# Optimization experiments

Hardware: AMD Instinct MI355X
Metric: run time of the kernel (lower is better)

Reference implementation:

```python
import jax, jax.numpy as jnp
import numpy as np


def setup_inputs() -> dict:
    key = jax.random.key(0)
    k_x, k1, k2, k3 = jax.random.split(key, 4)
    dim, hidden, out_dim = 4096, 8192, 4096
    x = jax.random.normal(k_x, (4, 2048, dim), dtype=jnp.float32)
    # VNNILinear initializes weight = randn(out, in) * 0.02
    w1 = jax.random.normal(k1, (hidden, dim), dtype=jnp.float32) * 0.02
    w2 = jax.random.normal(k2, (out_dim, hidden), dtype=jnp.float32) * 0.02
    w3 = jax.random.normal(k3, (hidden, dim), dtype=jnp.float32) * 0.02
    return {"x": x, "w1": w1, "w2": w2, "w3": w3}


def _quant_linear(x, w):
    """Emulate VNNILinear int8 weight-quantized matmul (inference path).

    Per-output-channel symmetric quant: scale = max|w_row| / 127,
    w_q = round(w / scale) in int8, y = x @ (w_q * scale).T.
    """
    w_max = jnp.clip(jnp.max(jnp.abs(w), axis=1, keepdims=True), 1e-6)  # [out,1]
    scale_w = w_max / 127.0
    w_q = jnp.round(w / scale_w).astype(jnp.int8)
    w_dq = w_q.astype(jnp.float32) * scale_w  # dequantized weight
    return jnp.einsum('bsd,hd->bsh', x, w_dq)


def reference(x, w1, w2, w3):
    # SwiGLU: w2( silu(w1(x)) * w3(x) ), all bias-free, int8 VNNI weight quant
    h = jax.nn.silu(_quant_linear(x, w1)) * _quant_linear(x, w3)  # [B,S,hidden]
    return _quant_linear(h, w2)  # [B,S,out_dim]
```

## Files before the change

### kernel.cpp

```cpp
#include <hip/hip_runtime.h>
#include <hip/hip_bf16.h>
#include <stdint.h>


typedef short bf16x8 __attribute__((ext_vector_type(8)));
typedef float f32x4  __attribute__((ext_vector_type(4)));
typedef float f32x16 __attribute__((ext_vector_type(16)));
typedef int   i32x4  __attribute__((ext_vector_type(4)));
typedef int   i32x16 __attribute__((ext_vector_type(16)));

__device__ __forceinline__ unsigned short f2bf(float f) {
  unsigned u = __builtin_bit_cast(unsigned, f);
  u += 0x7FFFu + ((u >> 16) & 1u);
  return (unsigned short)(u >> 16);
}

#define GLOAD_LDS16(gaddr, laddr)                                             \
  __builtin_amdgcn_global_load_lds(                                           \
      (const __attribute__((address_space(1))) void*)(gaddr),                 \
      (__attribute__((address_space(3))) void*)(laddr), 16, 0, 0)

#define FENCE()      asm volatile("" ::: "memory")
#define BAR()        __builtin_amdgcn_s_barrier()
#define WAIT_LGKM(n) asm volatile("s_waitcnt lgkmcnt(" #n ")" ::: "memory")
#define WAIT_VM8()   asm volatile("s_waitcnt vmcnt(8)" ::: "memory")
#define WAIT_VM4()   asm volatile("s_waitcnt vmcnt(4)" ::: "memory")
#define WAIT_VM0()   asm volatile("s_waitcnt vmcnt(0)" ::: "memory")
#define SFENCE()     __builtin_amdgcn_sched_barrier(0)
#define PRIO1()      __builtin_amdgcn_s_setprio(1)
#define PRIO0()      __builtin_amdgcn_s_setprio(0)


__global__ void quant_rows_i8_kernel(const float* __restrict__ w,
                                     char* __restrict__ q,
                                     float* __restrict__ scale, int cols,
                                     float clip) {
  const int row = blockIdx.x;
  const float* wr = w + (size_t)row * cols;
  char* qr = q + (size_t)row * cols;

  float m = 0.f;
  for (int c = threadIdx.x * 4; c < cols; c += blockDim.x * 4) {
    float4 v = *reinterpret_cast<const float4*>(wr + c);
    m = fmaxf(m, fmaxf(fmaxf(fabsf(v.x), fabsf(v.y)),
                       fmaxf(fabsf(v.z), fabsf(v.w))));
  }
#pragma unroll
  for (int off = 32; off; off >>= 1) m = fmaxf(m, __shfl_xor(m, off));
  __shared__ float smax[4];
  if ((threadIdx.x & 63) == 0) smax[threadIdx.x >> 6] = m;
  __syncthreads();
  m = fmaxf(fmaxf(smax[0], smax[1]), fmaxf(smax[2], smax[3]));

  const float s = fmaxf(m, clip) / 127.0f;
  if (threadIdx.x == 0) scale[row] = s;
  for (int c = threadIdx.x * 4; c < cols; c += blockDim.x * 4) {
    float4 v = *reinterpret_cast<const float4*>(wr + c);
    int b0 = (int)rintf(v.x / s), b1 = (int)rintf(v.y / s);
    int b2 = (int)rintf(v.z / s), b3 = (int)rintf(v.w / s);
    unsigned pk = (b0 & 0xff) | ((b1 & 0xff) << 8) | ((b2 & 0xff) << 16)
                  | ((b3 & 0xff) << 24);
    *reinterpret_cast<unsigned*>(qr + c) = pk;
  }
}

__global__ void quant_rows_bf16_kernel(const float* __restrict__ w,
                                       unsigned short* __restrict__ wq,
                                       int cols) {
  const int row = blockIdx.x;
  const float* wr = w + (size_t)row * cols;
  unsigned short* wqr = wq + (size_t)row * cols;

  float m = 0.f;
  for (int c = threadIdx.x * 4; c < cols; c += blockDim.x * 4) {
    float4 v = *reinterpret_cast<const float4*>(wr + c);
    m = fmaxf(m, fmaxf(fmaxf(fabsf(v.x), fabsf(v.y)),
                       fmaxf(fabsf(v.z), fabsf(v.w))));
  }
#pragma unroll
  for (int off = 32; off; off >>= 1) m = fmaxf(m, __shfl_xor(m, off));
  __shared__ float smax[4];
  if ((threadIdx.x & 63) == 0) smax[threadIdx.x >> 6] = m;
  __syncthreads();
  m = fmaxf(fmaxf(smax[0], smax[1]), fmaxf(smax[2], smax[3]));

  const float s = fmaxf(m, 1e-6f) / 127.0f;
  for (int c = threadIdx.x * 4; c < cols; c += blockDim.x * 4) {
    float4 v = *reinterpret_cast<const float4*>(wr + c);
    ushort4 o;
    o.x = f2bf(rintf(v.x / s) * s);
    o.y = f2bf(rintf(v.y / s) * s);
    o.z = f2bf(rintf(v.z / s) * s);
    o.w = f2bf(rintf(v.w / s) * s);
    *reinterpret_cast<ushort4*>(wqr + c) = o;
  }
}


__device__ __forceinline__ void xcd_swizzle(int& bx, int& by, int gx, int gy) {
  int nwg = gx * gy;
  int bid = by * gx + bx;
  int cpx = nwg >> 3;
  int s = (bid & 7) * cpx + (bid >> 3);
  by = s / gx;
  bx = s % gx;
}

__global__ __launch_bounds__(512, 2)
void gemm_i8_swiglu_kernel(const char* __restrict__ Aq,
                           const char* __restrict__ B1q,
                           const char* __restrict__ B3q,
                           const float* __restrict__ sx,
                           const float* __restrict__ sw1,
                           const float* __restrict__ sw3,
                           unsigned short* __restrict__ H,
                           int M, int N, int K) {
  __shared__ alignas(1024) char lds[131072];

  int bx = blockIdx.x, by = blockIdx.y;
  xcd_swizzle(bx, by, gridDim.x, gridDim.y);
  const int brow = by * 256, bcol = bx * 128;

  const int t = threadIdx.x, lane = t & 63, w = t >> 6;
  const int wr = w >> 2, wc = w & 3;
  const int l31 = lane & 31, hi = lane >> 5;
  const int NT = K >> 6;

  const int rS = t >> 2;
  const int gcS = ((t & 3) ^ ((t >> 3) & 3)) * 16;
  const char* srcA  = Aq  + (size_t)(brow + rS) * K + gcS;
  const char* srcB1 = B1q + (size_t)(bcol + rS) * K + gcS;
  const char* srcB3 = B3q + (size_t)(bcol + rS) * K + gcS;

#define STAGE_A(kt)                                                           \
  {                                                                           \
    const int s2 = ((kt) & 3) * 32768;                                        \
    const size_t ko = (size_t)(kt) * 64;                                      \
    GLOAD_LDS16(srcA + ko, lds + s2 + t * 16);                                \
    GLOAD_LDS16(srcA + (size_t)128 * K + ko, lds + s2 + 8192 + t * 16);       \
  }
#define STAGE_B(kt)                                                           \
  {                                                                           \
    const int s2 = ((kt) & 3) * 32768;                                        \
    const size_t ko = (size_t)(kt) * 64;                                      \
    GLOAD_LDS16(srcB1 + ko, lds + s2 + 16384 + t * 16);                       \
    GLOAD_LDS16(srcB3 + ko, lds + s2 + 24576 + t * 16);                       \
  }

  STAGE_A(0); STAGE_B(0);
  STAGE_A(1); STAGE_B(1);
  STAGE_A(2); STAGE_B(2);
  WAIT_VM8();
  FENCE(); BAR();

  const int sx2 = (l31 >> 1) & 3;
  const int aoff  = (wr * 128 + l31) * 64 + ((hi ^ sx2) * 16);
  const int boff1 = 16384 + (wc * 32 + l31) * 64 + ((hi ^ sx2) * 16);
  const int boff3 = boff1 + 8192;

  i32x16 acc[4][2] = {};
  i32x4 a0[4], b10, b30;
  i32x4 a1[4], b11, b31;

#pragma unroll
  for (int m = 0; m < 4; ++m)
    a0[m] = *reinterpret_cast<const i32x4*>(lds + aoff + m * 2048);
  b10 = *reinterpret_cast<const i32x4*>(lds + boff1);
  b30 = *reinterpret_cast<const i32x4*>(lds + boff3);

#define MFMA8(ar, b1r, b3r)                                                   \
  acc[0][0] = __builtin_amdgcn_mfma_i32_32x32x32_i8(ar[0], b1r, acc[0][0], 0, 0, 0); \
  acc[0][1] = __builtin_amdgcn_mfma_i32_32x32x32_i8(ar[0], b3r, acc[0][1], 0, 0, 0); \
  acc[1][0] = __builtin_amdgcn_mfma_i32_32x32x32_i8(ar[1], b1r, acc[1][0], 0, 0, 0); \
  acc[1][1] = __builtin_amdgcn_mfma_i32_32x32x32_i8(ar[1], b3r, acc[1][1], 0, 0, 0); \
  acc[2][0] = __builtin_amdgcn_mfma_i32_32x32x32_i8(ar[2], b1r, acc[2][0], 0, 0, 0); \
  acc[2][1] = __builtin_amdgcn_mfma_i32_32x32x32_i8(ar[2], b3r, acc[2][1], 0, 0, 0); \
  acc[3][0] = __builtin_amdgcn_mfma_i32_32x32x32_i8(ar[3], b1r, acc[3][0], 0, 0, 0); \
  acc[3][1] = __builtin_amdgcn_mfma_i32_32x32x32_i8(ar[3], b3r, acc[3][1], 0, 0, 0)

  int kb = 0;
  for (; kb < NT - 4; kb += 4) {
    const char* pA  = srcA  + (size_t)kb * 64;
    const char* pB1 = srcB1 + (size_t)kb * 64;
    const char* pB3 = srcB3 + (size_t)kb * 64;
#pragma unroll
    for (int s = 0; s < 4; ++s) {
      const char* sl = lds + s * 32768;
      const char* sn = lds + (((s + 1) & 3) * 32768);
      char* sp = lds + (((s + 3) & 3) * 32768);
      const int ko = (s + 3) * 64;

      a1[0] = *reinterpret_cast<const i32x4*>(sl + (aoff ^ 32));
      a1[1] = *reinterpret_cast<const i32x4*>(sl + (aoff ^ 32) + 2048);
      a1[2] = *reinterpret_cast<const i32x4*>(sl + (aoff ^ 32) + 4096);
      a1[3] = *reinterpret_cast<const i32x4*>(sl + (aoff ^ 32) + 6144);
      b11 = *reinterpret_cast<const i32x4*>(sl + (boff1 ^ 32));
      b31 = *reinterpret_cast<const i32x4*>(sl + (boff3 ^ 32));
      GLOAD_LDS16(pA + ko, sp + t * 16);
      GLOAD_LDS16(pA + (size_t)128 * K + ko, sp + 8192 + t * 16);
      WAIT_LGKM(6); SFENCE();
      PRIO1(); MFMA8(a0, b10, b30); PRIO0();

      GLOAD_LDS16(pB1 + ko, sp + 16384 + t * 16);
      GLOAD_LDS16(pB3 + ko, sp + 24576 + t * 16);
      WAIT_VM8();
      WAIT_LGKM(0);
      FENCE(); BAR();
      a0[0] = *reinterpret_cast<const i32x4*>(sn + aoff);
      a0[1] = *reinterpret_cast<const i32x4*>(sn + aoff + 2048);
      a0[2] = *reinterpret_cast<const i32x4*>(sn + aoff + 4096);
      a0[3] = *reinterpret_cast<const i32x4*>(sn + aoff + 6144);
      b10 = *reinterpret_cast<const i32x4*>(sn + boff1);
      b30 = *reinterpret_cast<const i32x4*>(sn + boff3);
      SFENCE();
      PRIO1(); MFMA8(a1, b11, b31); PRIO0();
    }
  }

  for (int k = kb; k < NT; ++k) {
    const char* sl = lds + (k & 3) * 32768;
    const bool pf = (k + 3 < NT);

    a1[0] = *reinterpret_cast<const i32x4*>(sl + (aoff ^ 32));
    a1[1] = *reinterpret_cast<const i32x4*>(sl + (aoff ^ 32) + 2048);
    a1[2] = *reinterpret_cast<const i32x4*>(sl + (aoff ^ 32) + 4096);
    a1[3] = *reinterpret_cast<const i32x4*>(sl + (aoff ^ 32) + 6144);
    b11 = *reinterpret_cast<const i32x4*>(sl + (boff1 ^ 32));
    b31 = *reinterpret_cast<const i32x4*>(sl + (boff3 ^ 32));
    if (pf) STAGE_A(k + 3);
    WAIT_LGKM(6); SFENCE();
    PRIO1(); MFMA8(a0, b10, b30); PRIO0();

    if (pf) {
      STAGE_B(k + 3);
      WAIT_VM8();
    } else if (k == NT - 3) {
      WAIT_VM4();
    } else if (k == NT - 2) {
      WAIT_VM0();
    }
    WAIT_LGKM(0);
    FENCE(); BAR();
    if (k + 1 < NT) {
      const char* sn = lds + ((k + 1) & 3) * 32768;
      a0[0] = *reinterpret_cast<const i32x4*>(sn + aoff);
      a0[1] = *reinterpret_cast<const i32x4*>(sn + aoff + 2048);
      a0[2] = *reinterpret_cast<const i32x4*>(sn + aoff + 4096);
      a0[3] = *reinterpret_cast<const i32x4*>(sn + aoff + 6144);
      b10 = *reinterpret_cast<const i32x4*>(sn + boff1);
      b30 = *reinterpret_cast<const i32x4*>(sn + boff3);
    }
    SFENCE();
    PRIO1(); MFMA8(a1, b11, b31); PRIO0();
  }
#undef MFMA8
#undef STAGE_A
#undef STAGE_B

  const int ocol = bcol + wc * 32 + l31;
  const int rowb = brow + wr * 128 + 4 * hi;
  const float sw1c = sw1[ocol], sw3c = sw3[ocol];
#pragma unroll
  for (int m = 0; m < 4; ++m) {
#pragma unroll
    for (int rq = 0; rq < 4; ++rq) {
      const int r0 = rowb + m * 32 + 8 * rq;
      const f32x4 sx4 = *reinterpret_cast<const f32x4*>(sx + r0);
#pragma unroll
      for (int j = 0; j < 4; ++j) {
        float y1 = (float)acc[m][0][rq * 4 + j] * (sx4[j] * sw1c);
        float y3 = (float)acc[m][1][rq * 4 + j] * (sx4[j] * sw3c);
        float hv = (y1 / (1.f + __expf(-y1))) * y3;
        H[(size_t)(r0 + j) * N + ocol] = f2bf(hv);
      }
    }
  }
}

__global__ __launch_bounds__(512, 2)
void gemm_bf16_kernel(const unsigned short* __restrict__ A,
                      const unsigned short* __restrict__ B,
                      float* __restrict__ C, int M, int N, int K) {
  __shared__ alignas(1024) unsigned short lds[65536];

  int bx = blockIdx.x, by = blockIdx.y;
  xcd_swizzle(bx, by, gridDim.x, gridDim.y);
  const int brow = by * 256, bcol = bx * 256;

  const int t = threadIdx.x, lane = t & 63, w = t >> 6;
  const int wr = w >> 2, wc = w & 3;
  const int l31 = lane & 31, hi = lane >> 5;
  const int NT = K >> 5;

  const int rS = t >> 2;
  const int cS = ((t & 3) ^ ((t >> 3) & 3)) * 8;
  const unsigned short* srcA = A + (size_t)(brow + rS) * K + cS;
  const unsigned short* srcB = B + (size_t)(bcol + rS) * K + cS;

#define STAGE_A(kt)                                                           \
  {                                                                           \
    const int s2 = ((kt) & 3) * 16384;                                        \
    const size_t ko = (size_t)(kt) * 32;                                      \
    GLOAD_LDS16(srcA + ko, &lds[s2 + t * 8]);                                 \
    GLOAD_LDS16(srcA + (size_t)128 * K + ko, &lds[s2 + 4096 + t * 8]);        \
  }
#define STAGE_B(kt)                                                           \
  {                                                                           \
    const int s2 = ((kt) & 3) * 16384;                                        \
    const size_t ko = (size_t)(kt) * 32;                                      \
    GLOAD_LDS16(srcB + ko, &lds[s2 + 8192 + t * 8]);                          \
    GLOAD_LDS16(srcB + (size_t)128 * K + ko, &lds[s2 + 12288 + t * 8]);       \
  }

  STAGE_A(0); STAGE_B(0);
  STAGE_A(1); STAGE_B(1);
  STAGE_A(2); STAGE_B(2);
  WAIT_VM8();
  FENCE(); BAR();

  const int sx2 = (l31 >> 1) & 3;
  const int aoff  = (wr * 128 + l31) * 32 + ((hi ^ sx2) * 8);
  const int boff0 = 8192 + (wc * 64 + l31) * 32 + ((hi ^ sx2) * 8);

  f32x16 acc[4][2] = {};
  bf16x8 a0[4], b00, b01;
  bf16x8 a1[4], b10, b11;

#pragma unroll
  for (int m = 0; m < 4; ++m)
    a0[m] = *reinterpret_cast<const bf16x8*>(&lds[aoff + m * 1024]);
  b00 = *reinterpret_cast<const bf16x8*>(&lds[boff0]);
  b01 = *reinterpret_cast<const bf16x8*>(&lds[boff0 + 1024]);

#define MFMA8(ar, bx0, bx1)                                                   \
  acc[0][0] = __builtin_amdgcn_mfma_f32_32x32x16_bf16(ar[0], bx0, acc[0][0], 0, 0, 0); \
  acc[0][1] = __builtin_amdgcn_mfma_f32_32x32x16_bf16(ar[0], bx1, acc[0][1], 0, 0, 0); \
  acc[1][0] = __builtin_amdgcn_mfma_f32_32x32x16_bf16(ar[1], bx0, acc[1][0], 0, 0, 0); \
  acc[1][1] = __builtin_amdgcn_mfma_f32_32x32x16_bf16(ar[1], bx1, acc[1][1], 0, 0, 0); \
  acc[2][0] = __builtin_amdgcn_mfma_f32_32x32x16_bf16(ar[2], bx0, acc[2][0], 0, 0, 0); \
  acc[2][1] = __builtin_amdgcn_mfma_f32_32x32x16_bf16(ar[2], bx1, acc[2][1], 0, 0, 0); \
  acc[3][0] = __builtin_amdgcn_mfma_f32_32x32x16_bf16(ar[3], bx0, acc[3][0], 0, 0, 0); \
  acc[3][1] = __builtin_amdgcn_mfma_f32_32x32x16_bf16(ar[3], bx1, acc[3][1], 0, 0, 0)

  int kb = 0;
  for (; kb < NT - 4; kb += 4) {
    const unsigned short* pA = srcA + (size_t)kb * 32;
    const unsigned short* pB = srcB + (size_t)kb * 32;
#pragma unroll
    for (int s = 0; s < 4; ++s) {
      const unsigned short* sl = lds + s * 16384;
      const unsigned short* sn = lds + (((s + 1) & 3) * 16384);
      unsigned short* sp = lds + (((s + 3) & 3) * 16384);
      const int ko = (s + 3) * 32;

      a1[0] = *reinterpret_cast<const bf16x8*>(sl + (aoff ^ 16));
      a1[1] = *reinterpret_cast<const bf16x8*>(sl + (aoff ^ 16) + 1024);
      a1[2] = *reinterpret_cast<const bf16x8*>(sl + (aoff ^ 16) + 2048);
      a1[3] = *reinterpret_cast<const bf16x8*>(sl + (aoff ^ 16) + 3072);
      b10 = *reinterpret_cast<const bf16x8*>(sl + (boff0 ^ 16));
      b11 = *reinterpret_cast<const bf16x8*>(sl + ((boff0 + 1024) ^ 16));
      GLOAD_LDS16(pA + ko, sp + t * 8);
      GLOAD_LDS16(pA + (size_t)128 * K + ko, sp + 4096 + t * 8);
      WAIT_LGKM(6); SFENCE();
      PRIO1(); MFMA8(a0, b00, b01); PRIO0();

      GLOAD_LDS16(pB + ko, sp + 8192 + t * 8);
      GLOAD_LDS16(pB + (size_t)128 * K + ko, sp + 12288 + t * 8);
      WAIT_VM8();
      WAIT_LGKM(0);
      FENCE(); BAR();
      a0[0] = *reinterpret_cast<const bf16x8*>(sn + aoff);
      a0[1] = *reinterpret_cast<const bf16x8*>(sn + aoff + 1024);
      a0[2] = *reinterpret_cast<const bf16x8*>(sn + aoff + 2048);
      a0[3] = *reinterpret_cast<const bf16x8*>(sn + aoff + 3072);
      b00 = *reinterpret_cast<const bf16x8*>(sn + boff0);
      b01 = *reinterpret_cast<const bf16x8*>(sn + boff0 + 1024);
      SFENCE();
      PRIO1(); MFMA8(a1, b10, b11); PRIO0();
    }
  }

  for (int k = kb; k < NT; ++k) {
    const unsigned short* sl = &lds[(k & 3) * 16384];
    const bool pf = (k + 3 < NT);

    a1[0] = *reinterpret_cast<const bf16x8*>(sl + (aoff ^ 16));
    a1[1] = *reinterpret_cast<const bf16x8*>(sl + (aoff ^ 16) + 1024);
    a1[2] = *reinterpret_cast<const bf16x8*>(sl + (aoff ^ 16) + 2048);
    a1[3] = *reinterpret_cast<const bf16x8*>(sl + (aoff ^ 16) + 3072);
    b10 = *reinterpret_cast<const bf16x8*>(sl + (boff0 ^ 16));
    b11 = *reinterpret_cast<const bf16x8*>(sl + ((boff0 + 1024) ^ 16));
    if (pf) STAGE_A(k + 3);
    WAIT_LGKM(6); SFENCE();
    PRIO1(); MFMA8(a0, b00, b01); PRIO0();

    if (pf) {
      STAGE_B(k + 3);
      WAIT_VM8();
    } else if (k == NT - 3) {
      WAIT_VM4();
    } else if (k == NT - 2) {
      WAIT_VM0();
    }
    WAIT_LGKM(0);
    FENCE(); BAR();
    if (k + 1 < NT) {
      const unsigned short* sn = &lds[((k + 1) & 3) * 16384];
      a0[0] = *reinterpret_cast<const bf16x8*>(sn + aoff);
      a0[1] = *reinterpret_cast<const bf16x8*>(sn + aoff + 1024);
      a0[2] = *reinterpret_cast<const bf16x8*>(sn + aoff + 2048);
      a0[3] = *reinterpret_cast<const bf16x8*>(sn + aoff + 3072);
      b00 = *reinterpret_cast<const bf16x8*>(sn + boff0);
      b01 = *reinterpret_cast<const bf16x8*>(sn + boff0 + 1024);
    }
    SFENCE();
    PRIO1(); MFMA8(a1, b10, b11); PRIO0();
  }
#undef MFMA8
#undef STAGE_A
#undef STAGE_B

  const int ocol = bcol + wc * 64 + l31;
  const int rowb = brow + wr * 128 + 4 * hi;
#pragma unroll
  for (int m = 0; m < 4; ++m)
#pragma unroll
    for (int n = 0; n < 2; ++n)
#pragma unroll
      for (int rq = 0; rq < 4; ++rq)
#pragma unroll
        for (int j = 0; j < 4; ++j)
          C[(size_t)(rowb + m * 32 + 8 * rq + j) * N + (ocol + n * 32)] =
              acc[m][n][rq * 4 + j];
}


extern "C" void kernel_launch(void* const* d_in, const int* in_sizes, int n_in,
                              void* d_out, int out_size, void* d_ws,
                              size_t ws_size, hipStream_t stream) {
  const float* x  = (const float*)d_in[0];
  const float* w1 = (const float*)d_in[1];
  const float* w2 = (const float*)d_in[2];
  const float* w3 = (const float*)d_in[3];
  float* out = (float*)d_out;

  const int DIM = 4096, HID = 8192;
  const int M = in_sizes[0] / DIM;

  char* xq  = (char*)d_ws;
  char* w1q = xq + (size_t)M * DIM;
  char* w3q = w1q + (size_t)HID * DIM;
  unsigned short* w2b = (unsigned short*)(w3q + (size_t)HID * DIM);
  unsigned short* h = w2b + (size_t)DIM * HID;
  float* sx  = (float*)(h + (size_t)M * HID);
  float* sw1 = sx + M;
  float* sw3 = sw1 + HID;

  quant_rows_i8_kernel<<<HID, 256, 0, stream>>>(w1, w1q, sw1, DIM, 1e-6f);
  quant_rows_i8_kernel<<<HID, 256, 0, stream>>>(w3, w3q, sw3, DIM, 1e-6f);
  quant_rows_i8_kernel<<<M, 256, 0, stream>>>(x, xq, sx, DIM, 1e-30f);
  quant_rows_bf16_kernel<<<DIM, 256, 0, stream>>>(w2, w2b, HID);

  gemm_i8_swiglu_kernel<<<dim3(HID / 128, M / 256), 512, 0, stream>>>(
      xq, w1q, w3q, sx, sw1, sw3, h, M, HID, DIM);
  gemm_bf16_kernel<<<dim3(DIM / 256, M / 256), 512, 0, stream>>>(
      h, w2b, out, M, DIM, HID);
}
```

Before: 1.235 ms.

## Hold quant rows in registers; balance GEMM staging loads across waves; stagger k-halves

The quantization kernels now load each row once into registers and reuse it for both the max pass and the quantize pass, removing the second global read of the fp32 weights and activations. In both GEMM kernels, odd and even waves swap which operand (A or B) they stage in the first and second prefetch slots, which evens out global-load issue between the two halves of each iteration. Odd waves also read the two k-halves of each LDS stage in the opposite order, likely to spread LDS bank traffic. The changes add template specialisation on fixed column counts and a per-wave branch in the staging code.

```diff
diff --git a/kernel.cpp b/kernel.cpp
--- a/kernel.cpp
+++ b/kernel.cpp
@@ -31,19 +31,21 @@
 #define PRIO0()      __builtin_amdgcn_s_setprio(0)
 
 
-__global__ void quant_rows_i8_kernel(const float* __restrict__ w,
-                                     char* __restrict__ q,
-                                     float* __restrict__ scale, int cols,
-                                     float clip) {
-  const int row = blockIdx.x;
-  const float* wr = w + (size_t)row * cols;
-  char* qr = q + (size_t)row * cols;
-
+template <int NCH>
+__global__ void quant_rows_i8_sp(const float* __restrict__ w,
+                                 char* __restrict__ q,
+                                 float* __restrict__ scale, float clip) {
+  const int cols = NCH * 1024;
+  const float* wr = w + (size_t)blockIdx.x * cols;
+  char* qr = q + (size_t)blockIdx.x * cols;
+
+  float4 v[NCH];
   float m = 0.f;
-  for (int c = threadIdx.x * 4; c < cols; c += blockDim.x * 4) {
-    float4 v = *reinterpret_cast<const float4*>(wr + c);
-    m = fmaxf(m, fmaxf(fmaxf(fabsf(v.x), fabsf(v.y)),
-                       fmaxf(fabsf(v.z), fabsf(v.w))));
+#pragma unroll
+  for (int j = 0; j < NCH; ++j) {
+    v[j] = *reinterpret_cast<const float4*>(wr + threadIdx.x * 4 + j * 1024);
+    m = fmaxf(m, fmaxf(fmaxf(fabsf(v[j].x), fabsf(v[j].y)),
+                       fmaxf(fabsf(v[j].z), fabsf(v[j].w))));
   }
 #pragma unroll
   for (int off = 32; off; off >>= 1) m = fmaxf(m, __shfl_xor(m, off));
@@ -53,29 +55,31 @@
   m = fmaxf(fmaxf(smax[0], smax[1]), fmaxf(smax[2], smax[3]));
 
   const float s = fmaxf(m, clip) / 127.0f;
-  if (threadIdx.x == 0) scale[row] = s;
-  for (int c = threadIdx.x * 4; c < cols; c += blockDim.x * 4) {
-    float4 v = *reinterpret_cast<const float4*>(wr + c);
-    int b0 = (int)rintf(v.x / s), b1 = (int)rintf(v.y / s);
-    int b2 = (int)rintf(v.z / s), b3 = (int)rintf(v.w / s);
+  if (threadIdx.x == 0) scale[blockIdx.x] = s;
+#pragma unroll
+  for (int j = 0; j < NCH; ++j) {
+    int b0 = (int)rintf(v[j].x / s), b1 = (int)rintf(v[j].y / s);
+    int b2 = (int)rintf(v[j].z / s), b3 = (int)rintf(v[j].w / s);
     unsigned pk = (b0 & 0xff) | ((b1 & 0xff) << 8) | ((b2 & 0xff) << 16)
                   | ((b3 & 0xff) << 24);
-    *reinterpret_cast<unsigned*>(qr + c) = pk;
-  }
-}
-
-__global__ void quant_rows_bf16_kernel(const float* __restrict__ w,
-                                       unsigned short* __restrict__ wq,
-                                       int cols) {
-  const int row = blockIdx.x;
-  const float* wr = w + (size_t)row * cols;
-  unsigned short* wqr = wq + (size_t)row * cols;
-
+    *reinterpret_cast<unsigned*>(qr + threadIdx.x * 4 + j * 1024) = pk;
+  }
+}
+
+template <int NCH>
+__global__ void quant_rows_bf16_sp(const float* __restrict__ w,
+                                   unsigned short* __restrict__ wq) {
+  const int cols = NCH * 1024;
+  const float* wr = w + (size_t)blockIdx.x * cols;
+  unsigned short* wqr = wq + (size_t)blockIdx.x * cols;
+
+  float4 v[NCH];
   float m = 0.f;
-  for (int c = threadIdx.x * 4; c < cols; c += blockDim.x * 4) {
-    float4 v = *reinterpret_cast<const float4*>(wr + c);
-    m = fmaxf(m, fmaxf(fmaxf(fabsf(v.x), fabsf(v.y)),
-                       fmaxf(fabsf(v.z), fabsf(v.w))));
+#pragma unroll
+  for (int j = 0; j < NCH; ++j) {
+    v[j] = *reinterpret_cast<const float4*>(wr + threadIdx.x * 4 + j * 1024);
+    m = fmaxf(m, fmaxf(fmaxf(fabsf(v[j].x), fabsf(v[j].y)),
+                       fmaxf(fabsf(v[j].z), fabsf(v[j].w))));
   }
 #pragma unroll
   for (int off = 32; off; off >>= 1) m = fmaxf(m, __shfl_xor(m, off));
@@ -85,14 +89,14 @@
   m = fmaxf(fmaxf(smax[0], smax[1]), fmaxf(smax[2], smax[3]));
 
   const float s = fmaxf(m, 1e-6f) / 127.0f;
-  for (int c = threadIdx.x * 4; c < cols; c += blockDim.x * 4) {
-    float4 v = *reinterpret_cast<const float4*>(wr + c);
+#pragma unroll
+  for (int j = 0; j < NCH; ++j) {
     ushort4 o;
-    o.x = f2bf(rintf(v.x / s) * s);
-    o.y = f2bf(rintf(v.y / s) * s);
-    o.z = f2bf(rintf(v.z / s) * s);
-    o.w = f2bf(rintf(v.w / s) * s);
-    *reinterpret_cast<ushort4*>(wqr + c) = o;
+    o.x = f2bf(rintf(v[j].x / s) * s);
+    o.y = f2bf(rintf(v[j].y / s) * s);
+    o.z = f2bf(rintf(v[j].z / s) * s);
+    o.w = f2bf(rintf(v[j].w / s) * s);
+    *reinterpret_cast<ushort4*>(wqr + threadIdx.x * 4 + j * 1024) = o;
   }
 }
 
@@ -124,6 +128,7 @@
   const int t = threadIdx.x, lane = t & 63, w = t >> 6;
   const int wr = w >> 2, wc = w & 3;
   const int l31 = lane & 31, hi = lane >> 5;
+  const bool wodd = (w & 1);
   const int NT = K >> 6;
 
   const int rS = t >> 2;
@@ -132,24 +137,29 @@
   const char* srcB1 = B1q + (size_t)(bcol + rS) * K + gcS;
   const char* srcB3 = B3q + (size_t)(bcol + rS) * K + gcS;
 
-#define STAGE_A(kt)                                                           \
-  {                                                                           \
-    const int s2 = ((kt) & 3) * 32768;                                        \
-    const size_t ko = (size_t)(kt) * 64;                                      \
-    GLOAD_LDS16(srcA + ko, lds + s2 + t * 16);                                \
-    GLOAD_LDS16(srcA + (size_t)128 * K + ko, lds + s2 + 8192 + t * 16);       \
-  }
-#define STAGE_B(kt)                                                           \
-  {                                                                           \
-    const int s2 = ((kt) & 3) * 32768;                                        \
-    const size_t ko = (size_t)(kt) * 64;                                      \
-    GLOAD_LDS16(srcB1 + ko, lds + s2 + 16384 + t * 16);                       \
-    GLOAD_LDS16(srcB3 + ko, lds + s2 + 24576 + t * 16);                       \
-  }
-
-  STAGE_A(0); STAGE_B(0);
-  STAGE_A(1); STAGE_B(1);
-  STAGE_A(2); STAGE_B(2);
+#define STAGE_P1(pA_, pB1_, pB3_, sp, ko)                                     \
+  if (!wodd) {                                                                \
+    GLOAD_LDS16((pA_) + (ko), (sp) + t * 16);                                 \
+    GLOAD_LDS16((pA_) + (size_t)128 * K + (ko), (sp) + 8192 + t * 16);        \
+  } else {                                                                    \
+    GLOAD_LDS16((pB1_) + (ko), (sp) + 16384 + t * 16);                        \
+    GLOAD_LDS16((pB3_) + (ko), (sp) + 24576 + t * 16);                        \
+  }
+#define STAGE_P2(pA_, pB1_, pB3_, sp, ko)                                     \
+  if (wodd) {                                                                 \
+    GLOAD_LDS16((pA_) + (ko), (sp) + t * 16);                                 \
+    GLOAD_LDS16((pA_) + (size_t)128 * K + (ko), (sp) + 8192 + t * 16);        \
+  } else {                                                                    \
+    GLOAD_LDS16((pB1_) + (ko), (sp) + 16384 + t * 16);                        \
+    GLOAD_LDS16((pB3_) + (ko), (sp) + 24576 + t * 16);                        \
+  }
+
+  STAGE_P1(srcA, srcB1, srcB3, lds, 0);
+  STAGE_P2(srcA, srcB1, srcB3, lds, 0);
+  STAGE_P1(srcA, srcB1, srcB3, lds + 32768, (size_t)64);
+  STAGE_P2(srcA, srcB1, srcB3, lds + 32768, (size_t)64);
+  STAGE_P1(srcA, srcB1, srcB3, lds + 65536, (size_t)128);
+  STAGE_P2(srcA, srcB1, srcB3, lds + 65536, (size_t)128);
   WAIT_VM8();
   FENCE(); BAR();
 
@@ -157,6 +167,8 @@
   const int aoff  = (wr * 128 + l31) * 64 + ((hi ^ sx2) * 16);
   const int boff1 = 16384 + (wc * 32 + l31) * 64 + ((hi ^ sx2) * 16);
   const int boff3 = boff1 + 8192;
+  const int kx0 = wodd ? 32 : 0;
+  const int kx1 = kx0 ^ 32;
 
   i32x16 acc[4][2] = {};
   i32x4 a0[4], b10, b30;
@@ -164,9 +176,9 @@
 
 #pragma unroll
   for (int m = 0; m < 4; ++m)
-    a0[m] = *reinterpret_cast<const i32x4*>(lds + aoff + m * 2048);
-  b10 = *reinterpret_cast<const i32x4*>(lds + boff1);
-  b30 = *reinterpret_cast<const i32x4*>(lds + boff3);
+    a0[m] = *reinterpret_cast<const i32x4*>(lds + (aoff ^ kx0) + m * 2048);
+  b10 = *reinterpret_cast<const i32x4*>(lds + (boff1 ^ kx0));
+  b30 = *reinterpret_cast<const i32x4*>(lds + (boff3 ^ kx0));
 
 #define MFMA8(ar, b1r, b3r)                                                   \
   acc[0][0] = __builtin_amdgcn_mfma_i32_32x32x32_i8(ar[0], b1r, acc[0][0], 0, 0, 0); \
@@ -190,28 +202,26 @@
       char* sp = lds + (((s + 3) & 3) * 32768);
       const int ko = (s + 3) * 64;
 
-      a1[0] = *reinterpret_cast<const i32x4*>(sl + (aoff ^ 32));
-      a1[1] = *reinterpret_cast<const i32x4*>(sl + (aoff ^ 32) + 2048);
-      a1[2] = *reinterpret_cast<const i32x4*>(sl + (aoff ^ 32) + 4096);
-      a1[3] = *reinterpret_cast<const i32x4*>(sl + (aoff ^ 32) + 6144);
-      b11 = *reinterpret_cast<const i32x4*>(sl + (boff1 ^ 32));
-      b31 = *reinterpret_cast<const i32x4*>(sl + (boff3 ^ 32));
-      GLOAD_LDS16(pA + ko, sp + t * 16);
-      GLOAD_LDS16(pA + (size_t)128 * K + ko, sp + 8192 + t * 16);
+      a1[0] = *reinterpret_cast<const i32x4*>(sl + (aoff ^ kx1));
+      a1[1] = *reinterpret_cast<const i32x4*>(sl + (aoff ^ kx1) + 2048);
+      a1[2] = *reinterpret_cast<const i32x4*>(sl + (aoff ^ kx1) + 4096);
+      a1[3] = *reinterpret_cast<const i32x4*>(sl + (aoff ^ kx1) + 6144);
+      b11 = *reinterpret_cast<const i32x4*>(sl + (boff1 ^ kx1));
+      b31 = *reinterpret_cast<const i32x4*>(sl + (boff3 ^ kx1));
+      STAGE_P1(pA, pB1, pB3, sp, ko);
       WAIT_LGKM(6); SFENCE();
       PRIO1(); MFMA8(a0, b10, b30); PRIO0();
 
-      GLOAD_LDS16(pB1 + ko, sp + 16384 + t * 16);
-      GLOAD_LDS16(pB3 + ko, sp + 24576 + t * 16);
+      STAGE_P2(pA, pB1, pB3, sp, ko);
       WAIT_VM8();
       WAIT_LGKM(0);
       FENCE(); BAR();
-      a0[0] = *reinterpret_cast<const i32x4*>(sn + aoff);
-      a0[1] = *reinterpret_cast<const i32x4*>(sn + aoff + 2048);
-      a0[2] = *reinterpret_cast<const i32x4*>(sn + aoff + 4096);
-      a0[3] = *reinterpret_cast<const i32x4*>(sn + aoff + 6144);
-      b10 = *reinterpret_cast<const i32x4*>(sn + boff1);
-      b30 = *reinterpret_cast<const i32x4*>(sn + boff3);
+      a0[0] = *reinterpret_cast<const i32x4*>(sn + (aoff ^ kx0));
+      a0[1] = *reinterpret_cast<const i32x4*>(sn + (aoff ^ kx0) + 2048);
+      a0[2] = *reinterpret_cast<const i32x4*>(sn + (aoff ^ kx0) + 4096);
+      a0[3] = *reinterpret_cast<const i32x4*>(sn + (aoff ^ kx0) + 6144);
+      b10 = *reinterpret_cast<const i32x4*>(sn + (boff1 ^ kx0));
+      b30 = *reinterpret_cast<const i32x4*>(sn + (boff3 ^ kx0));
       SFENCE();
       PRIO1(); MFMA8(a1, b11, b31); PRIO0();
     }
@@ -221,18 +231,22 @@
     const char* sl = lds + (k & 3) * 32768;
     const bool pf = (k + 3 < NT);
 
-    a1[0] = *reinterpret_cast<const i32x4*>(sl + (aoff ^ 32));
-    a1[1] = *reinterpret_cast<const i32x4*>(sl + (aoff ^ 32) + 2048);
-    a1[2] = *reinterpret_cast<const i32x4*>(sl + (aoff ^ 32) + 4096);
-    a1[3] = *reinterpret_cast<const i32x4*>(sl + (aoff ^ 32) + 6144);
-    b11 = *reinterpret_cast<const i32x4*>(sl + (boff1 ^ 32));
-    b31 = *reinterpret_cast<const i32x4*>(sl + (boff3 ^ 32));
-    if (pf) STAGE_A(k + 3);
+    a1[0] = *reinterpret_cast<const i32x4*>(sl + (aoff ^ kx1));
+    a1[1] = *reinterpret_cast<const i32x4*>(sl + (aoff ^ kx1) + 2048);
+    a1[2] = *reinterpret_cast<const i32x4*>(sl + (aoff ^ kx1) + 4096);
+    a1[3] = *reinterpret_cast<const i32x4*>(sl + (aoff ^ kx1) + 6144);
+    b11 = *reinterpret_cast<const i32x4*>(sl + (boff1 ^ kx1));
+    b31 = *reinterpret_cast<const i32x4*>(sl + (boff3 ^ kx1));
+    if (pf) {
+      char* sp = lds + (((k + 3) & 3) * 32768);
+      STAGE_P1(srcA, srcB1, srcB3, sp, (size_t)(k + 3) * 64);
+    }
     WAIT_LGKM(6); SFENCE();
     PRIO1(); MFMA8(a0, b10, b30); PRIO0();
 
     if (pf) {
-      STAGE_B(k + 3);
+      char* sp = lds + (((k + 3) & 3) * 32768);
+      STAGE_P2(srcA, srcB1, srcB3, sp, (size_t)(k + 3) * 64);
       WAIT_VM8();
     } else if (k == NT - 3) {
       WAIT_VM4();
@@ -243,19 +257,19 @@
     FENCE(); BAR();
     if (k + 1 < NT) {
       const char* sn = lds + ((k + 1) & 3) * 32768;
-      a0[0] = *reinterpret_cast<const i32x4*>(sn + aoff);
-      a0[1] = *reinterpret_cast<const i32x4*>(sn + aoff + 2048);
-      a0[2] = *reinterpret_cast<const i32x4*>(sn + aoff + 4096);
-      a0[3] = *reinterpret_cast<const i32x4*>(sn + aoff + 6144);
-      b10 = *reinterpret_cast<const i32x4*>(sn + boff1);
-      b30 = *reinterpret_cast<const i32x4*>(sn + boff3);
+      a0[0] = *reinterpret_cast<const i32x4*>(sn + (aoff ^ kx0));
+      a0[1] = *reinterpret_cast<const i32x4*>(sn + (aoff ^ kx0) + 2048);
+      a0[2] = *reinterpret_cast<const i32x4*>(sn + (aoff ^ kx0) + 4096);
+      a0[3] = *reinterpret_cast<const i32x4*>(sn + (aoff ^ kx0) + 6144);
+      b10 = *reinterpret_cast<const i32x4*>(sn + (boff1 ^ kx0));
+      b30 = *reinterpret_cast<const i32x4*>(sn + (boff3 ^ kx0));
     }
     SFENCE();
     PRIO1(); MFMA8(a1, b11, b31); PRIO0();
   }
 #undef MFMA8
-#undef STAGE_A
-#undef STAGE_B
+#undef STAGE_P1
+#undef STAGE_P2
 
   const int ocol = bcol + wc * 32 + l31;
   const int rowb = brow + wr * 128 + 4 * hi;
@@ -290,6 +304,7 @@
   const int t = threadIdx.x, lane = t & 63, w = t >> 6;
   const int wr = w >> 2, wc = w & 3;
   const int l31 = lane & 31, hi = lane >> 5;
+  const bool wodd = (w & 1);
   const int NT = K >> 5;
 
   const int rS = t >> 2;
@@ -297,30 +312,38 @@
   const unsigned short* srcA = A + (size_t)(brow + rS) * K + cS;
   const unsigned short* srcB = B + (size_t)(bcol + rS) * K + cS;
 
-#define STAGE_A(kt)                                                           \
-  {                                                                           \
-    const int s2 = ((kt) & 3) * 16384;                                        \
-    const size_t ko = (size_t)(kt) * 32;                                      \
-    GLOAD_LDS16(srcA + ko, &lds[s2 + t * 8]);                                 \
-    GLOAD_LDS16(srcA + (size_t)128 * K + ko, &lds[s2 + 4096 + t * 8]);        \
-  }
-#define STAGE_B(kt)                                                           \
-  {                                                                           \
-    const int s2 = ((kt) & 3) * 16384;                                        \
-    const size_t ko = (size_t)(kt) * 32;                                      \
-    GLOAD_LDS16(srcB + ko, &lds[s2 + 8192 + t * 8]);                          \
-    GLOAD_LDS16(srcB + (size_t)128 * K + ko, &lds[s2 + 12288 + t * 8]);       \
-  }
-
-  STAGE_A(0); STAGE_B(0);
-  STAGE_A(1); STAGE_B(1);
-  STAGE_A(2); STAGE_B(2);
+#define STAGE_P1(pA_, pB_, sp, ko)                                            \
+  if (!wodd) {                                                                \
+    GLOAD_LDS16((pA_) + (ko), (sp) + t * 8);                                  \
+    GLOAD_LDS16((pA_) + (size_t)128 * K + (ko), (sp) + 4096 + t * 8);         \
+  } else {                                                                    \
+    GLOAD_LDS16((pB_) + (ko), (sp) + 8192 + t * 8);                           \
+    GLOAD_LDS16((pB_) + (size_t)128 * K + (ko), (sp) + 12288 + t * 8);        \
+  }
+#define STAGE_P2(pA_, pB_, sp, ko)                                            \
+  if (wodd) {                                                                 \
+    GLOAD_LDS16((pA_) + (ko), (sp) + t * 8);                                  \
+    GLOAD_LDS16((pA_) + (size_t)128 * K + (ko), (sp) + 4096 + t * 8);         \
+  } else {                                                                    \
+    GLOAD_LDS16((pB_) + (ko), (sp) + 8192 + t * 8);                           \
+    GLOAD_LDS16((pB_) + (size_t)128 * K + (ko), (sp) + 12288 + t * 8);        \
+  }
+
+  STAGE_P1(srcA, srcB, lds, 0);
+  STAGE_P2(srcA, srcB, lds, 0);
+  STAGE_P1(srcA, srcB, lds + 16384, (size_t)32);
+  STAGE_P2(srcA, srcB, lds + 16384, (size_t)32);
+  STAGE_P1(srcA, srcB, lds + 32768, (size_t)64);
+  STAGE_P2(srcA, srcB, lds + 32768, (size_t)64);
   WAIT_VM8();
   FENCE(); BAR();
 
   const int sx2 = (l31 >> 1) & 3;
   const int aoff  = (wr * 128 + l31) * 32 + ((hi ^ sx2) * 8);
   const int boff0 = 8192 + (wc * 64 + l31) * 32 + ((hi ^ sx2) * 8);
+  const int boff1b = boff0 + 1024;
+  const int kx0 = wodd ? 16 : 0;
+  const int kx1 = kx0 ^ 16;
 
   f32x16 acc[4][2] = {};
   bf16x8 a0[4], b00, b01;
@@ -328,9 +351,9 @@
 
 #pragma unroll
   for (int m = 0; m < 4; ++m)
-    a0[m] = *reinterpret_cast<const bf16x8*>(&lds[aoff + m * 1024]);
-  b00 = *reinterpret_cast<const bf16x8*>(&lds[boff0]);
-  b01 = *reinterpret_cast<const bf16x8*>(&lds[boff0 + 1024]);
+    a0[m] = *reinterpret_cast<const bf16x8*>(&lds[(aoff ^ kx0) + m * 1024]);
+  b00 = *reinterpret_cast<const bf16x8*>(&lds[boff0 ^ kx0]);
+  b01 = *reinterpret_cast<const bf16x8*>(&lds[boff1b ^ kx0]);
 
 #define MFMA8(ar, bx0, bx1)                                                   \
   acc[0][0] = __builtin_amdgcn_mfma_f32_32x32x16_bf16(ar[0], bx0, acc[0][0], 0, 0, 0); \
@@ -353,28 +376,26 @@
       unsigned short* sp = lds + (((s + 3) & 3) * 16384);
       const int ko = (s + 3) * 32;
 
-      a1[0] = *reinterpret_cast<const bf16x8*>(sl + (aoff ^ 16));
-      a1[1] = *reinterpret_cast<const bf16x8*>(sl + (aoff ^ 16) + 1024);
-      a1[2] = *reinterpret_cast<const bf16x8*>(sl + (aoff ^ 16) + 2048);
-      a1[3] = *reinterpret_cast<const bf16x8*>(sl + (aoff ^ 16) + 3072);
-      b10 = *reinterpret_cast<const bf16x8*>(sl + (boff0 ^ 16));
-      b11 = *reinterpret_cast<const bf16x8*>(sl + ((boff0 + 1024) ^ 16));
-      GLOAD_LDS16(pA + ko, sp + t * 8);
-      GLOAD_LDS16(pA + (size_t)128 * K + ko, sp + 4096 + t * 8);
+      a1[0] = *reinterpret_cast<const bf16x8*>(sl + (aoff ^ kx1));
+      a1[1] = *reinterpret_cast<const bf16x8*>(sl + (aoff ^ kx1) + 1024);
+      a1[2] = *reinterpret_cast<const bf16x8*>(sl + (aoff ^ kx1) + 2048);
+      a1[3] = *reinterpret_cast<const bf16x8*>(sl + (aoff ^ kx1) + 3072);
+      b10 = *reinterpret_cast<const bf16x8*>(sl + (boff0 ^ kx1));
+      b11 = *reinterpret_cast<const bf16x8*>(sl + (boff1b ^ kx1));
+      STAGE_P1(pA, pB, sp, ko);
       WAIT_LGKM(6); SFENCE();
       PRIO1(); MFMA8(a0, b00, b01); PRIO0();
 
-      GLOAD_LDS16(pB + ko, sp + 8192 + t * 8);
-      GLOAD_LDS16(pB + (size_t)128 * K + ko, sp + 12288 + t * 8);
+      STAGE_P2(pA, pB, sp, ko);
       WAIT_VM8();
       WAIT_LGKM(0);
       FENCE(); BAR();
-      a0[0] = *reinterpret_cast<const bf16x8*>(sn + aoff);
-      a0[1] = *reinterpret_cast<const bf16x8*>(sn + aoff + 1024);
-      a0[2] = *reinterpret_cast<const bf16x8*>(sn + aoff + 2048);
-      a0[3] = *reinterpret_cast<const bf16x8*>(sn + aoff + 3072);
-      b00 = *reinterpret_cast<const bf16x8*>(sn + boff0);
-      b01 = *reinterpret_cast<const bf16x8*>(sn + boff0 + 1024);
+      a0[0] = *reinterpret_cast<const bf16x8*>(sn + (aoff ^ kx0));
+      a0[1] = *reinterpret_cast<const bf16x8*>(sn + (aoff ^ kx0) + 1024);
+      a0[2] = *reinterpret_cast<const bf16x8*>(sn + (aoff ^ kx0) + 2048);
+      a0[3] = *reinterpret_cast<const bf16x8*>(sn + (aoff ^ kx0) + 3072);
+      b00 = *reinterpret_cast<const bf16x8*>(sn + (boff0 ^ kx0));
+      b01 = *reinterpret_cast<const bf16x8*>(sn + (boff1b ^ kx0));
       SFENCE();
       PRIO1(); MFMA8(a1, b10, b11); PRIO0();
     }
@@ -384,18 +405,22 @@
     const unsigned short* sl = &lds[(k & 3) * 16384];
     const bool pf = (k + 3 < NT);
 
-    a1[0] = *reinterpret_cast<const bf16x8*>(sl + (aoff ^ 16));
-    a1[1] = *reinterpret_cast<const bf16x8*>(sl + (aoff ^ 16) + 1024);
-    a1[2] = *reinterpret_cast<const bf16x8*>(sl + (aoff ^ 16) + 2048);
-    a1[3] = *reinterpret_cast<const bf16x8*>(sl + (aoff ^ 16) + 3072);
-    b10 = *reinterpret_cast<const bf16x8*>(sl + (boff0 ^ 16));
-    b11 = *reinterpret_cast<const bf16x8*>(sl + ((boff0 + 1024) ^ 16));
-    if (pf) STAGE_A(k + 3);
+    a1[0] = *reinterpret_cast<const bf16x8*>(sl + (aoff ^ kx1));
+    a1[1] = *reinterpret_cast<const bf16x8*>(sl + (aoff ^ kx1) + 1024);
+    a1[2] = *reinterpret_cast<const bf16x8*>(sl + (aoff ^ kx1) + 2048);
+    a1[3] = *reinterpret_cast<const bf16x8*>(sl + (aoff ^ kx1) + 3072);
+    b10 = *reinterpret_cast<const bf16x8*>(sl + (boff0 ^ kx1));
+    b11 = *reinterpret_cast<const bf16x8*>(sl + (boff1b ^ kx1));
+    if (pf) {
+      unsigned short* sp = lds + (((k + 3) & 3) * 16384);
+      STAGE_P1(srcA, srcB, sp, (size_t)(k + 3) * 32);
+    }
     WAIT_LGKM(6); SFENCE();
     PRIO1(); MFMA8(a0, b00, b01); PRIO0();
 
     if (pf) {
-      STAGE_B(k + 3);
+      unsigned short* sp = lds + (((k + 3) & 3) * 16384);
+      STAGE_P2(srcA, srcB, sp, (size_t)(k + 3) * 32);
       WAIT_VM8();
     } else if (k == NT - 3) {
       WAIT_VM4();
@@ -406,19 +431,19 @@
     FENCE(); BAR();
     if (k + 1 < NT) {
       const unsigned short* sn = &lds[((k + 1) & 3) * 16384];
-      a0[0] = *reinterpret_cast<const bf16x8*>(sn + aoff);
-      a0[1] = *reinterpret_cast<const bf16x8*>(sn + aoff + 1024);
-      a0[2] = *reinterpret_cast<const bf16x8*>(sn + aoff + 2048);
-      a0[3] = *reinterpret_cast<const bf16x8*>(sn + aoff + 3072);
-      b00 = *reinterpret_cast<const bf16x8*>(sn + boff0);
-      b01 = *reinterpret_cast<const bf16x8*>(sn + boff0 + 1024);
+      a0[0] = *reinterpret_cast<const bf16x8*>(sn + (aoff ^ kx0));
+      a0[1] = *reinterpret_cast<const bf16x8*>(sn + (aoff ^ kx0) + 1024);
+      a0[2] = *reinterpret_cast<const bf16x8*>(sn + (aoff ^ kx0) + 2048);
+      a0[3] = *reinterpret_cast<const bf16x8*>(sn + (aoff ^ kx0) + 3072);
+      b00 = *reinterpret_cast<const bf16x8*>(sn + (boff0 ^ kx0));
+      b01 = *reinterpret_cast<const bf16x8*>(sn + (boff1b ^ kx0));
     }
     SFENCE();
     PRIO1(); MFMA8(a1, b10, b11); PRIO0();
   }
 #undef MFMA8
-#undef STAGE_A
-#undef STAGE_B
+#undef STAGE_P1
+#undef STAGE_P2
 
   const int ocol = bcol + wc * 64 + l31;
   const int rowb = brow + wr * 128 + 4 * hi;
@@ -456,10 +481,10 @@
   float* sw1 = sx + M;
   float* sw3 = sw1 + HID;
 
-  quant_rows_i8_kernel<<<HID, 256, 0, stream>>>(w1, w1q, sw1, DIM, 1e-6f);
-  quant_rows_i8_kernel<<<HID, 256, 0, stream>>>(w3, w3q, sw3, DIM, 1e-6f);
-  quant_rows_i8_kernel<<<M, 256, 0, stream>>>(x, xq, sx, DIM, 1e-30f);
-  quant_rows_bf16_kernel<<<DIM, 256, 0, stream>>>(w2, w2b, HID);
+  quant_rows_i8_sp<4><<<HID, 256, 0, stream>>>(w1, w1q, sw1, 1e-6f);
+  quant_rows_i8_sp<4><<<HID, 256, 0, stream>>>(w3, w3q, sw3, 1e-6f);
+  quant_rows_i8_sp<4><<<M, 256, 0, stream>>>(x, xq, sx, 1e-30f);
+  quant_rows_bf16_sp<8><<<DIM, 256, 0, stream>>>(w2, w2b);
 
   gemm_i8_swiglu_kernel<<<dim3(HID / 128, M / 256), 512, 0, stream>>>(
       xq, w1q, w3q, sx, sw1, sw3, h, M, HID, DIM);
```

New measurement: 1.217 ms, median of 2. No clear change (-1.5%).
